# Kernel tuning notes

Measured on AMD Instinct MI355X. Metric: run time of the kernel, lower is better.

The kernel has to match this reference:

```python
import jax, jax.numpy as jnp
import numpy as np

D = 512
SEG_LEN = 128
RCL = 32          # right_context_length
K = 31            # depthwise kernel size
STATE = K - 1     # state_size = 30
U = 2048          # utterance length = 16 segments * SEG_LEN
R = 512           # right context length total = 16 * RCL
B = 32
EPS = 1e-5


def layer_norm(x, g, b):
    m = jnp.mean(x, axis=-1, keepdims=True)
    v = jnp.mean((x - m) ** 2, axis=-1, keepdims=True)
    return (x - m) * jax.lax.rsqrt(v + EPS) * g + b


def dwconv(x, w, b):
    # x: [N, D, T], w: [D, 1, K] depthwise, b: [D]
    y = jax.lax.conv_general_dilated(
        x, w, window_strides=(1,), padding='VALID',
        dimension_numbers=('NCH', 'OIH', 'NCH'), feature_group_count=x.shape[1])
    return y + b[None, :, None]


def setup_inputs() -> dict:
    key = jax.random.key(0)
    ks = jax.random.split(key, 8)
    s = 0.02
    return {
        'utterance': jax.random.normal(ks[0], (U, B, D), jnp.float32),
        'right_context': jax.random.normal(ks[1], (R, B, D), jnp.float32),
        'state': jnp.zeros((B, D, STATE), jnp.float32),
        'ln1_g': jnp.ones((D,), jnp.float32),
        'ln1_b': jnp.zeros((D,), jnp.float32),
        'w1': jax.random.normal(ks[2], (2 * D, D), jnp.float32) * s,
        'b1': jnp.zeros((2 * D,), jnp.float32),
        'conv_w': jax.random.normal(ks[3], (D, 1, K), jnp.float32) * s,
        'conv_b': jnp.zeros((D,), jnp.float32),
        'ln2_g': jnp.ones((D,), jnp.float32),
        'ln2_b': jnp.zeros((D,), jnp.float32),
        'w2': jax.random.normal(ks[4], (D, D), jnp.float32) * s,
        'b2': jnp.zeros((D,), jnp.float32),
    }


def reference(utterance, right_context, state, ln1_g, ln1_b, w1, b1,
              conv_w, conv_b, ln2_g, ln2_b, w2, b2):
    inp = jnp.concatenate((right_context, utterance), axis=0)  # [R+U, B, D]
    # pre_conv: LayerNorm -> Linear(D, 2D) -> GLU
    x = layer_norm(inp, ln1_g, ln1_b) @ w1.T + b1
    a, g = jnp.split(x, 2, axis=-1)
    x = a * jax.nn.sigmoid(g)                                  # [R+U, B, D]
    x_rc, x_utt = x[:R], x[R:]
    x_utt_t = jnp.transpose(x_utt, (1, 2, 0))                  # [B, D, U]
    state_x = jnp.concatenate([state, x_utt_t], axis=2)        # [B, D, STATE+U]
    conv_utt = jnp.transpose(dwconv(state_x, conv_w, conv_b), (2, 0, 1))  # [U, B, D]
    # right-context block conv (vectorized segment splicing)
    S = R // RCL
    su = jnp.transpose(state_x, (2, 0, 1))                     # [STATE+U, B, D]
    rc_seg = x_rc.reshape(S, RCL, B, D).transpose(0, 2, 1, 3).reshape(S * B, RCL, D)
    offs = (jnp.arange(S) + 1) * SEG_LEN                       # start = end - STATE
    idx = offs[:, None] + jnp.arange(STATE)[None, :]           # [S, STATE]
    pads = su[idx]                                             # [S, STATE, B, D]
    pads = pads.transpose(0, 2, 1, 3).reshape(S * B, STATE, D)
    block = jnp.transpose(jnp.concatenate([pads, rc_seg], axis=1), (0, 2, 1))  # [S*B, D, STATE+RCL]
    conv_rc = dwconv(block, conv_w, conv_b)                    # [S*B, D, RCL]
    conv_rc = conv_rc.reshape(S, B, D, RCL).transpose(0, 3, 1, 2).reshape(R, B, D)
    y = jnp.concatenate([conv_rc, conv_utt], axis=0)           # [R+U, B, D]
    # post_conv: LayerNorm -> SiLU -> Linear -> (dropout p=0) ; residual add
    out = jax.nn.silu(layer_norm(y, ln2_g, ln2_b)) @ w2.T + b2 + inp
    new_state = state_x[:, :, -STATE:]
    return out[R:], out[:R], new_state
```

## Files before the change

kernel.cpp:

```cpp
#include <hip/hip_runtime.h>


#define Dm 512
#define STATE 30
#define Uu 2048
#define Rr 512
#define Bb 32
#define Tt 2560
#define MROWS 81920

typedef unsigned short u16;
typedef unsigned int u32;
typedef __attribute__((ext_vector_type(8))) __bf16 bf16x8;
typedef __attribute__((ext_vector_type(4))) float f32x4;

__device__ __forceinline__ u16 f2bf(float x) {
  u32 u = __float_as_uint(x);
  u += 0x7fff + ((u >> 16) & 1);
  return (u16)(u >> 16);
}
__device__ __forceinline__ float bf2f(u16 h) {
  return __uint_as_float((u32)h << 16);
}
__device__ __forceinline__ void load_lds16(const void* g, void* l) {
  __builtin_amdgcn_global_load_lds(
      (const __attribute__((address_space(1))) void*)g,
      (__attribute__((address_space(3))) void*)l, 16, 0, 0);
}

__global__ __launch_bounds__(256, 4) void k_cast(const float* __restrict__ src,
                                                 u16* __restrict__ dst, int n) {
  int i = (blockIdx.x * 256 + threadIdx.x) * 4;
  if (i >= n) return;
  float4 v = *(const float4*)(src + i);
  u32 lo = (u32)f2bf(v.x) | ((u32)f2bf(v.y) << 16);
  u32 hi = (u32)f2bf(v.z) | ((u32)f2bf(v.w) << 16);
  *(uint2*)(dst + i) = make_uint2(lo, hi);
}

__global__ __launch_bounds__(256, 4) void k_wt(const float* __restrict__ cw,
                                               float* __restrict__ cwT) {
  int i = blockIdx.x * 256 + threadIdx.x;
  if (i >= 31 * 512) return;
  int k = i >> 9, d = i & 511;
  cwT[i] = cw[d * 31 + k];
}

__global__ __launch_bounds__(256, 4) void k_ln1(const float* __restrict__ utt,
                                                const float* __restrict__ rc,
                                                const float* __restrict__ g,
                                                const float* __restrict__ b,
                                                u16* __restrict__ out) {
  int wid = threadIdx.x >> 6, lane = threadIdx.x & 63;
  long row = (long)blockIdx.x * 4 + wid;
  const float* src = (row < (long)Rr * Bb) ? rc + row * Dm
                                           : utt + (row - (long)Rr * Bb) * Dm;
  int d0 = lane * 8;
  float4 v0 = *(const float4*)(src + d0);
  float4 v1 = *(const float4*)(src + d0 + 4);
  float s = v0.x + v0.y + v0.z + v0.w + v1.x + v1.y + v1.z + v1.w;
  float ss = v0.x * v0.x + v0.y * v0.y + v0.z * v0.z + v0.w * v0.w +
             v1.x * v1.x + v1.y * v1.y + v1.z * v1.z + v1.w * v1.w;
#pragma unroll
  for (int off = 1; off < 64; off <<= 1) {
    s += __shfl_xor(s, off);
    ss += __shfl_xor(ss, off);
  }
  float mean = s * (1.f / 512.f);
  float var = ss * (1.f / 512.f) - mean * mean;
  float rstd = rsqrtf(var + 1e-5f);
  float4 g0 = *(const float4*)(g + d0);
  float4 g1 = *(const float4*)(g + d0 + 4);
  float4 b0 = *(const float4*)(b + d0);
  float4 b1v = *(const float4*)(b + d0 + 4);
  float o[8];
  o[0] = (v0.x - mean) * rstd * g0.x + b0.x;
  o[1] = (v0.y - mean) * rstd * g0.y + b0.y;
  o[2] = (v0.z - mean) * rstd * g0.z + b0.z;
  o[3] = (v0.w - mean) * rstd * g0.w + b0.w;
  o[4] = (v1.x - mean) * rstd * g1.x + b1v.x;
  o[5] = (v1.y - mean) * rstd * g1.y + b1v.y;
  o[6] = (v1.z - mean) * rstd * g1.z + b1v.z;
  o[7] = (v1.w - mean) * rstd * g1.w + b1v.w;
  u32 p[4];
#pragma unroll
  for (int i = 0; i < 4; ++i)
    p[i] = (u32)f2bf(o[2 * i]) | ((u32)f2bf(o[2 * i + 1]) << 16);
  *(uint4*)(out + row * Dm + d0) = make_uint4(p[0], p[1], p[2], p[3]);
}

__global__ __launch_bounds__(256, 2) void k_gemm1(const u16* __restrict__ A,
                                                  const u16* __restrict__ Wb,
                                                  const float* __restrict__ b1,
                                                  u16* __restrict__ X) {
  __shared__ __align__(16) u16 sA[128 * 64], sBa[128 * 64], sBg[128 * 64];
  int tid = threadIdx.x;
  int bid = blockIdx.x;
  int bm = bid >> 2, nt = bid & 3;
  long arow0 = (long)bm * 128;
  int ncol0 = nt * 128;
  int lane = tid & 63, wid = tid >> 6;
  int wm = (wid >> 1) * 64, wn = (wid & 1) * 64;
  int lr = lane & 15, kg = lane >> 4;
  int l7 = lr & 7;

  f32x4 acc_a[4][4], acc_g[4][4];
#pragma unroll
  for (int i = 0; i < 4; ++i)
#pragma unroll
    for (int j = 0; j < 4; ++j) {
      acc_a[i][j] = (f32x4)0.f;
      acc_g[i][j] = (f32x4)0.f;
    }

  for (int k0 = 0; k0 < 512; k0 += 64) {
#pragma unroll
    for (int i = 0; i < 4; ++i) {
      int c = i * 256 + tid;
      int r = c >> 3;
      int col = ((c & 7) ^ (r & 7)) * 8;
      load_lds16(A + (arow0 + r) * 512 + k0 + col, &sA[c * 8]);
      load_lds16(Wb + (long)(ncol0 + r) * 512 + k0 + col, &sBa[c * 8]);
      load_lds16(Wb + (long)(512 + ncol0 + r) * 512 + k0 + col, &sBg[c * 8]);
    }
    __syncthreads();
#pragma unroll
    for (int kf = 0; kf < 2; ++kf) {
      int u = (kf * 4 + kg) ^ l7;
      bf16x8 av[4], bav[4], bgv[4];
#pragma unroll
      for (int i = 0; i < 4; ++i) {
        av[i] = *(const bf16x8*)&sA[(wm + i * 16 + lr) * 64 + u * 8];
        bav[i] = *(const bf16x8*)&sBa[(wn + i * 16 + lr) * 64 + u * 8];
        bgv[i] = *(const bf16x8*)&sBg[(wn + i * 16 + lr) * 64 + u * 8];
      }
#pragma unroll
      for (int mi = 0; mi < 4; ++mi)
#pragma unroll
        for (int ni = 0; ni < 4; ++ni) {
          acc_a[mi][ni] = __builtin_amdgcn_mfma_f32_16x16x32_bf16(
              av[mi], bav[ni], acc_a[mi][ni], 0, 0, 0);
          acc_g[mi][ni] = __builtin_amdgcn_mfma_f32_16x16x32_bf16(
              av[mi], bgv[ni], acc_g[mi][ni], 0, 0, 0);
        }
    }
    __syncthreads();
  }
  int mg = kg * 4;
#pragma unroll
  for (int mi = 0; mi < 4; ++mi) {
#pragma unroll
    for (int ni = 0; ni < 4; ++ni) {
      int ncol = ncol0 + wn + ni * 16 + lr;
      float ba = b1[ncol], bg = b1[512 + ncol];
#pragma unroll
      for (int rgi = 0; rgi < 4; ++rgi) {
        long row = arow0 + wm + mi * 16 + mg + rgi;
        float a = acc_a[mi][ni][rgi] + ba;
        float gg = acc_g[mi][ni][rgi] + bg;
        float val = a / (1.f + __expf(-gg));
        X[row * 512 + ncol] = f2bf(val);
      }
    }
  }
}

__global__ __launch_bounds__(256, 2) void k_conv_ln2(
    const u16* __restrict__ X, const float* __restrict__ state,
    const float* __restrict__ cwT, const float* __restrict__ cb,
    const float* __restrict__ g2, const float* __restrict__ bt2,
    u16* __restrict__ Z) {
  __shared__ __align__(16) u16 stX[46 * 512];
  __shared__ float stats[16][2];
  float* ys = (float*)stX;

  int t = threadIdx.x;
  int d0 = t * 2;
  int tile = blockIdx.x, b = blockIdx.y;
  int wv = t >> 6, ln = t & 63;

  float w0[31], w1[31];
#pragma unroll
  for (int k = 0; k < 31; ++k) {
    float2 wp = *(const float2*)&cwT[k * 512 + d0];
    w0[k] = wp.x;
    w1[k] = wp.y;
  }
  float a0[16], a1[16];
  {
    float2 cb2 = *(const float2*)&cb[d0];
#pragma unroll
    for (int r = 0; r < 16; ++r) {
      a0[r] = cb2.x;
      a1[r] = cb2.y;
    }
  }

  auto step = [&](int j, float x0, float x1) {
#pragma unroll
    for (int r = 0; r < 16; ++r) {
      int k = j - r;
      if (k >= 0 && k < 31) {
        a0[r] += x0 * w0[k];
        a1[r] += x1 * w1[k];
      }
    }
  };

  const u16* Xb = X + (long)b * 512;

  if (tile >= 2) {
    if (tile < 128) {
      long base = (long)Rr + tile * 16 - 30;
      for (int r = wv; r < 46; r += 4)
        load_lds16(Xb + (base + r) * 16384 + ln * 8, &stX[r * 512 + ln * 8]);
    } else if (tile < 144) {
      int s = tile - 128;
      for (int r = wv; r < 46; r += 4) {
        long trow = (r < 30) ? ((long)Rr + 128 * (s + 1) - 30 + r)
                             : ((long)32 * s + r - 30);
        load_lds16(Xb + trow * 16384 + ln * 8, &stX[r * 512 + ln * 8]);
      }
    } else {
      int s = tile - 144;
      for (int r = wv; r < 46; r += 4) {
        long trow = (r < 14) ? ((long)Rr + 128 * (s + 1) - 14 + r)
                             : ((long)32 * s + r - 14);
        load_lds16(Xb + trow * 16384 + ln * 8, &stX[r * 512 + ln * 8]);
      }
    }
    __syncthreads();
#pragma unroll
    for (int j = 0; j < 46; ++j) {
      u32 xx = *(const u32*)&stX[j * 512 + d0];
      float x0 = __uint_as_float(xx << 16);
      float x1 = __uint_as_float(xx & 0xffff0000u);
      step(j, x0, x1);
      if ((j & 7) == 7) __builtin_amdgcn_sched_barrier(0);
    }
  } else {
    long t0 = (long)tile * 16;
    const float* st0 = state + ((long)b * 512 + d0) * 30;
    const float* st1 = st0 + 30;
    const u16* Xc = Xb + d0;
#pragma unroll
    for (int j = 0; j < 46; ++j) {
      long tj = t0 - 30 + j;
      float x0, x1;
      if (tj < 0) {
        x0 = st0[tj + 30];
        x1 = st1[tj + 30];
      } else {
        u32 xx = *(const u32*)&Xc[((long)Rr + tj) * 16384];
        x0 = __uint_as_float(xx << 16);
        x1 = __uint_as_float(xx & 0xffff0000u);
      }
      step(j, x0, x1);
      if ((j & 15) == 15) __builtin_amdgcn_sched_barrier(0);
    }
  }

  __syncthreads();
#pragma unroll
  for (int r = 0; r < 16; ++r) {
    float2 v = make_float2(a0[r], a1[r]);
    *(float2*)&ys[r * 512 + d0] = v;
  }
  __syncthreads();

#pragma unroll
  for (int rr = 0; rr < 4; ++rr) {
    int r = wv * 4 + rr;
    float4 va = *(const float4*)&ys[r * 512 + ln * 8];
    float4 vb = *(const float4*)&ys[r * 512 + ln * 8 + 4];
    float s = va.x + va.y + va.z + va.w + vb.x + vb.y + vb.z + vb.w;
    float ss = va.x * va.x + va.y * va.y + va.z * va.z + va.w * va.w +
               vb.x * vb.x + vb.y * vb.y + vb.z * vb.z + vb.w * vb.w;
#pragma unroll
    for (int off = 1; off < 64; off <<= 1) {
      s += __shfl_xor(s, off);
      ss += __shfl_xor(ss, off);
    }
    if (ln == 0) {
      float mean = s * (1.f / 512.f);
      float var = ss * (1.f / 512.f) - mean * mean;
      stats[r][0] = mean;
      stats[r][1] = rsqrtf(var + 1e-5f);
    }
  }
  __syncthreads();

  float2 gg = *(const float2*)&g2[d0];
  float2 bb = *(const float2*)&bt2[d0];
  long orow0;
  if (tile < 128) {
    orow0 = ((long)Rr + tile * 16) * Bb + b;
  } else if (tile < 144) {
    orow0 = (long)(32 * (tile - 128)) * Bb + b;
  } else {
    orow0 = (long)(32 * (tile - 144) + 16) * Bb + b;
  }
#pragma unroll
  for (int r = 0; r < 16; ++r) {
    float mean = stats[r][0], rstd = stats[r][1];
    float y0 = (a0[r] - mean) * rstd * gg.x + bb.x;
    float y1 = (a1[r] - mean) * rstd * gg.y + bb.y;
    float z0 = y0 / (1.f + __expf(-y0));
    float z1 = y1 / (1.f + __expf(-y1));
    u32 pz = (u32)f2bf(z0) | ((u32)f2bf(z1) << 16);
    *(u32*)&Z[(orow0 + (long)r * Bb) * 512 + d0] = pz;
  }
}

__global__ __launch_bounds__(256, 2) void k_gemm2(const u16* __restrict__ A,
                                                  const u16* __restrict__ Wb,
                                                  const float* __restrict__ b2,
                                                  const float* __restrict__ utt,
                                                  const float* __restrict__ rc,
                                                  float* __restrict__ out) {
  __shared__ __align__(16) u16 smem[2 * 128 * 64];
  u16* sA = smem;
  u16* sB = smem + 128 * 64;
  float* tile = (float*)smem;

  int tid = threadIdx.x;
  int bid = blockIdx.x;
  int bm = bid >> 2, nt = bid & 3;
  long arow0 = (long)bm * 128;
  int ncol0 = nt * 128;
  int lane = tid & 63, wid = tid >> 6;
  int wm = (wid >> 1) * 64, wn = (wid & 1) * 64;
  int lr = lane & 15, kg = lane >> 4;
  int l7 = lr & 7;

  f32x4 acc[4][4];
#pragma unroll
  for (int i = 0; i < 4; ++i)
#pragma unroll
    for (int j = 0; j < 4; ++j) acc[i][j] = (f32x4)0.f;

  for (int k0 = 0; k0 < 512; k0 += 64) {
#pragma unroll
    for (int i = 0; i < 4; ++i) {
      int c = i * 256 + tid;
      int r = c >> 3;
      int col = ((c & 7) ^ (r & 7)) * 8;
      load_lds16(A + (arow0 + r) * 512 + k0 + col, &sA[c * 8]);
      load_lds16(Wb + (long)(ncol0 + r) * 512 + k0 + col, &sB[c * 8]);
    }
    __syncthreads();
#pragma unroll
    for (int kf = 0; kf < 2; ++kf) {
      int u = (kf * 4 + kg) ^ l7;
      bf16x8 av[4], bv[4];
#pragma unroll
      for (int i = 0; i < 4; ++i) {
        av[i] = *(const bf16x8*)&sA[(wm + i * 16 + lr) * 64 + u * 8];
        bv[i] = *(const bf16x8*)&sB[(wn + i * 16 + lr) * 64 + u * 8];
      }
#pragma unroll
      for (int mi = 0; mi < 4; ++mi)
#pragma unroll
        for (int ni = 0; ni < 4; ++ni)
          acc[mi][ni] = __builtin_amdgcn_mfma_f32_16x16x32_bf16(
              av[mi], bv[ni], acc[mi][ni], 0, 0, 0);
    }
    __syncthreads();
  }

  float b2v[4];
#pragma unroll
  for (int ni = 0; ni < 4; ++ni) b2v[ni] = b2[ncol0 + wn + ni * 16 + lr];
  int mg = kg * 4;

#pragma unroll
  for (int p = 0; p < 2; ++p) {
    if ((wid >> 1) == p) {
#pragma unroll
      for (int mi = 0; mi < 4; ++mi)
#pragma unroll
        for (int ni = 0; ni < 4; ++ni)
#pragma unroll
          for (int rgi = 0; rgi < 4; ++rgi) {
            int rl = mi * 16 + mg + rgi;
            int cl = wn + ni * 16 + lr;
            tile[rl * 128 + (cl ^ ((rl & 3) << 3))] = acc[mi][ni][rgi] + b2v[ni];
          }
    }
    __syncthreads();
    long rowbase = arow0 + p * 64;
    bool is_rc = rowbase < 16384;
#pragma unroll
    for (int rr = 0; rr < 8; ++rr) {
      int idx = rr * 256 + tid;
      int r = idx >> 5, c4 = (idx & 31) << 2;
      float4 v = *(const float4*)&tile[r * 128 + (c4 ^ ((r & 3) << 3))];
      long row = rowbase + r;
      const float* src;
      float* dst;
      if (is_rc) {
        src = rc + row * 512;
        dst = out + 33554432 + row * 512;
      } else {
        src = utt + (row - 16384) * 512;
        dst = out + (row - 16384) * 512;
      }
      float4 rv = *(const float4*)&src[ncol0 + c4];
      v.x += rv.x; v.y += rv.y; v.z += rv.z; v.w += rv.w;
      *(float4*)&dst[ncol0 + c4] = v;
    }
    __syncthreads();
  }
}

__global__ __launch_bounds__(256, 4) void k_state(const u16* __restrict__ X,
                                                  float* __restrict__ out) {
  int i = blockIdx.x * 256 + threadIdx.x;
  if (i >= 491520) return;
  int j = i % 30;
  int rest = i / 30;
  int d = rest & 511;
  int b = rest >> 9;
  out[41943040 + i] = bf2f(X[((long)(2530 + j) * Bb + b) * 512 + d]);
}

extern "C" void kernel_launch(void* const* d_in, const int* in_sizes, int n_in,
                              void* d_out, int out_size, void* d_ws, size_t ws_size,
                              hipStream_t stream) {
  const float* utt = (const float*)d_in[0];
  const float* rc = (const float*)d_in[1];
  const float* state = (const float*)d_in[2];
  const float* ln1g = (const float*)d_in[3];
  const float* ln1b = (const float*)d_in[4];
  const float* w1 = (const float*)d_in[5];
  const float* b1 = (const float*)d_in[6];
  const float* cw = (const float*)d_in[7];
  const float* cb = (const float*)d_in[8];
  const float* ln2g = (const float*)d_in[9];
  const float* ln2b = (const float*)d_in[10];
  const float* w2 = (const float*)d_in[11];
  const float* b2 = (const float*)d_in[12];
  float* out = (float*)d_out;

  char* ws = (char*)d_ws;
  u16* w1b = (u16*)ws;
  u16* w2b = (u16*)(ws + (1 << 20));
  float* cwT = (float*)(ws + (1 << 20) + (1 << 19));
  u16* lnx = (u16*)(ws + (1 << 20) + (1 << 19) + (1 << 16));
  u16* xbuf = lnx + (size_t)MROWS * Dm;

  k_cast<<<512, 256, 0, stream>>>(w1, w1b, 1024 * 512);
  k_cast<<<256, 256, 0, stream>>>(w2, w2b, 512 * 512);
  k_wt<<<62, 256, 0, stream>>>(cw, cwT);
  k_ln1<<<MROWS / 4, 256, 0, stream>>>(utt, rc, ln1g, ln1b, lnx);
  k_gemm1<<<2560, 256, 0, stream>>>(lnx, w1b, b1, xbuf);
  k_conv_ln2<<<dim3(160, 32), 256, 0, stream>>>(xbuf, state, cwT, cb, ln2g, ln2b, lnx);
  k_gemm2<<<2560, 256, 0, stream>>>(lnx, w2b, b2, utt, rc, out);
  k_state<<<1920, 256, 0, stream>>>(xbuf, out);
}
```

Measured before the change: 365.3 us.

## Double-buffer GEMM1 with half-K staging, larger 256-row tiles and interleaved a/g weights

The GLU projection GEMM is restructured to use 512-thread blocks covering 256 rows by 128 output columns. Global-to-LDS loads are double-buffered in two K-halves with explicit vmcnt waits, so the next tile's loads overlap the current MFMAs. The a and gate weight rows are interleaved into one B tile, so each wave's accumulators hold matching a/g column pairs. MFMA sections also get raised scheduling priority. The change uses more LDS (128KB per block) and more accumulator registers, which may reduce occupancy.

```diff
diff --git a/kernel.cpp b/kernel.cpp
--- a/kernel.cpp
+++ b/kernel.cpp
@@ -89,77 +89,87 @@
   *(uint4*)(out + row * Dm + d0) = make_uint4(p[0], p[1], p[2], p[3]);
 }
 
-__global__ __launch_bounds__(256, 2) void k_gemm1(const u16* __restrict__ A,
+__global__ __launch_bounds__(512, 2) void k_gemm1(const u16* __restrict__ A,
                                                   const u16* __restrict__ Wb,
                                                   const float* __restrict__ b1,
                                                   u16* __restrict__ X) {
-  __shared__ __align__(16) u16 sA[128 * 64], sBa[128 * 64], sBg[128 * 64];
+  __shared__ __align__(16) u16 sA[2][2][8192], sB[2][2][8192];
   int tid = threadIdx.x;
   int bid = blockIdx.x;
   int bm = bid >> 2, nt = bid & 3;
-  long arow0 = (long)bm * 128;
+  long arow0 = (long)bm * 256;
   int ncol0 = nt * 128;
   int lane = tid & 63, wid = tid >> 6;
-  int wm = (wid >> 1) * 64, wn = (wid & 1) * 64;
+  int wr = wid >> 2, wc = wid & 3;
   int lr = lane & 15, kg = lane >> 4;
-  int l7 = lr & 7;
-
-  f32x4 acc_a[4][4], acc_g[4][4];
-#pragma unroll
-  for (int i = 0; i < 4; ++i)
-#pragma unroll
-    for (int j = 0; j < 4; ++j) {
-      acc_a[i][j] = (f32x4)0.f;
-      acc_g[i][j] = (f32x4)0.f;
-    }
-
-  for (int k0 = 0; k0 < 512; k0 += 64) {
-#pragma unroll
-    for (int i = 0; i < 4; ++i) {
-      int c = i * 256 + tid;
-      int r = c >> 3;
-      int col = ((c & 7) ^ (r & 7)) * 8;
-      load_lds16(A + (arow0 + r) * 512 + k0 + col, &sA[c * 8]);
-      load_lds16(Wb + (long)(ncol0 + r) * 512 + k0 + col, &sBa[c * 8]);
-      load_lds16(Wb + (long)(512 + ncol0 + r) * 512 + k0 + col, &sBg[c * 8]);
-    }
-    __syncthreads();
+  int l3 = lr & 3;
+
+  f32x4 acc[8][4];
+#pragma unroll
+  for (int i = 0; i < 8; ++i)
+#pragma unroll
+    for (int j = 0; j < 4; ++j) acc[i][j] = (f32x4)0.f;
+
+  auto STAGE_HALF = [&](int buf, int k0, int kh) {
+#pragma unroll
+    for (int q = 0; q < 2; ++q) {
+      int c2 = q * 512 + tid;
+      int r = c2 >> 2, ch = c2 & 3;
+      int colu = k0 + kh * 32 + ((ch ^ (r & 3)) << 3);
+      load_lds16(A + (arow0 + r) * 512 + colu, &sA[buf][kh][r * 32 + ch * 8]);
+      int h = (r >> 5) & 1;
+      int wcol = ncol0 + ((r >> 6) << 5) + (r & 31);
+      load_lds16(Wb + (long)(h * 512 + wcol) * 512 + colu, &sB[buf][kh][r * 32 + ch * 8]);
+    }
+  };
+
+  STAGE_HALF(0, 0, 0);
+  STAGE_HALF(0, 0, 1);
+
+  for (int t = 0; t < 8; ++t) {
+    int cur = t & 1;
 #pragma unroll
     for (int kf = 0; kf < 2; ++kf) {
-      int u = (kf * 4 + kg) ^ l7;
-      bf16x8 av[4], bav[4], bgv[4];
-#pragma unroll
-      for (int i = 0; i < 4; ++i) {
-        av[i] = *(const bf16x8*)&sA[(wm + i * 16 + lr) * 64 + u * 8];
-        bav[i] = *(const bf16x8*)&sBa[(wn + i * 16 + lr) * 64 + u * 8];
-        bgv[i] = *(const bf16x8*)&sBg[(wn + i * 16 + lr) * 64 + u * 8];
-      }
-#pragma unroll
-      for (int mi = 0; mi < 4; ++mi)
-#pragma unroll
-        for (int ni = 0; ni < 4; ++ni) {
-          acc_a[mi][ni] = __builtin_amdgcn_mfma_f32_16x16x32_bf16(
-              av[mi], bav[ni], acc_a[mi][ni], 0, 0, 0);
-          acc_g[mi][ni] = __builtin_amdgcn_mfma_f32_16x16x32_bf16(
-              av[mi], bgv[ni], acc_g[mi][ni], 0, 0, 0);
-        }
-    }
-    __syncthreads();
-  }
-  int mg = kg * 4;
-#pragma unroll
-  for (int mi = 0; mi < 4; ++mi) {
-#pragma unroll
-    for (int ni = 0; ni < 4; ++ni) {
-      int ncol = ncol0 + wn + ni * 16 + lr;
-      float ba = b1[ncol], bg = b1[512 + ncol];
-#pragma unroll
-      for (int rgi = 0; rgi < 4; ++rgi) {
-        long row = arow0 + wm + mi * 16 + mg + rgi;
-        float a = acc_a[mi][ni][rgi] + ba;
-        float gg = acc_g[mi][ni][rgi] + bg;
-        float val = a / (1.f + __expf(-gg));
-        X[row * 512 + ncol] = f2bf(val);
+      if (t == 7 && kf == 1)
+        asm volatile("s_waitcnt vmcnt(0)" ::: "memory");
+      else
+        asm volatile("s_waitcnt vmcnt(4)" ::: "memory");
+      __builtin_amdgcn_sched_barrier(0);
+      __builtin_amdgcn_s_barrier();
+      __builtin_amdgcn_sched_barrier(0);
+      if (t < 7) STAGE_HALF(cur ^ 1, (t + 1) * 64, kf);
+      bf16x8 av[8], bv[4];
+#pragma unroll
+      for (int i = 0; i < 8; ++i)
+        av[i] = *(const bf16x8*)
+            &sA[cur][kf][(wr * 128 + i * 16 + lr) * 32 + ((kg ^ l3) << 3)];
+#pragma unroll
+      for (int i = 0; i < 4; ++i)
+        bv[i] = *(const bf16x8*)
+            &sB[cur][kf][(wc * 64 + i * 16 + lr) * 32 + ((kg ^ l3) << 3)];
+      __builtin_amdgcn_s_setprio(1);
+#pragma unroll
+      for (int mi = 0; mi < 8; ++mi)
+#pragma unroll
+        for (int ni = 0; ni < 4; ++ni)
+          acc[mi][ni] = __builtin_amdgcn_mfma_f32_16x16x32_bf16(
+              av[mi], bv[ni], acc[mi][ni], 0, 0, 0);
+      __builtin_amdgcn_s_setprio(0);
+    }
+  }
+
+#pragma unroll
+  for (int ni = 0; ni < 2; ++ni) {
+    int col = ncol0 + wc * 32 + ni * 16 + lr;
+    float ba = b1[col], bg = b1[512 + col];
+#pragma unroll
+    for (int mi = 0; mi < 8; ++mi) {
+#pragma unroll
+      for (int rg = 0; rg < 4; ++rg) {
+        long row = arow0 + wr * 128 + mi * 16 + kg * 4 + rg;
+        float a = acc[mi][ni][rg] + ba;
+        float gg = acc[mi][ni + 2][rg] + bg;
+        X[row * 512 + col] = f2bf(a / (1.f + __expf(-gg)));
       }
     }
   }
@@ -453,7 +463,7 @@
   k_cast<<<256, 256, 0, stream>>>(w2, w2b, 512 * 512);
   k_wt<<<62, 256, 0, stream>>>(cw, cwT);
   k_ln1<<<MROWS / 4, 256, 0, stream>>>(utt, rc, ln1g, ln1b, lnx);
-  k_gemm1<<<2560, 256, 0, stream>>>(lnx, w1b, b1, xbuf);
+  k_gemm1<<<1280, 512, 0, stream>>>(lnx, w1b, b1, xbuf);
   k_conv_ln2<<<dim3(160, 32), 256, 0, stream>>>(xbuf, state, cwT, cb, ln2g, ln2b, lnx);
   k_gemm2<<<2560, 256, 0, stream>>>(lnx, w2b, b2, utt, rc, out);
   k_state<<<1920, 256, 0, stream>>>(xbuf, out);
```

Measured after the change: 381.3 us. 1.04x slower.
